# Kernel tuning notes

Measured on AMD Instinct MI355X. Metric: run time of the kernel, lower is better.

The kernel has to match this reference:

```python
import jax, jax.numpy as jnp
import numpy as np


def setup_inputs() -> dict:
    key = jax.random.key(0)
    k1, k2, k3 = jax.random.split(key, 3)
    N, S = 65536, 128  # rays, samples per ray
    # t: sorted sample distances along each ray (near=2.0, far=6.0 typical NeRF bounds)
    t = jnp.sort(jax.random.uniform(k1, (N, S, 1), jnp.float32, 2.0, 6.0), axis=-2)
    # sigma: non-negative densities (post-ReLU/softplus output of NerfDensity)
    sigma = jax.random.uniform(k2, (N, S, 1), jnp.float32, 0.0, 2.0)
    # color: RGB in [0,1] (post-sigmoid output of NerfColor)
    color = jax.random.uniform(k3, (N, S, 3), jnp.float32, 0.0, 1.0)
    return {"t": t, "sigma": sigma, "color": color}


def integrate_ray(t, sigma, color, infinite=False):
    # t, sigma: [N, S, 1]; color: [N, S, 3]
    dt = t[..., 1:, :] - t[..., :-1, :]                      # [N, S-1, 1]
    last = 1e10 * jnp.ones_like(dt[..., 0:1, :]) if infinite else jnp.zeros_like(dt[..., 0:1, :])
    dt = jnp.concatenate((dt, last), axis=-2)                # [N, S, 1]
    sdt = sigma * dt                                         # [N, S, 1]
    Ti = jnp.exp(-jnp.cumsum(sdt, axis=-2))[..., 0:-1, :]    # transmittance, shifted
    Ti = jnp.concatenate((jnp.ones_like(Ti[..., 0:1, :]), Ti), axis=-2)
    alpha = 1.0 - jnp.exp(-sdt)
    wi = Ti * alpha                                          # [N, S, 1]
    return ((wi * color).sum(axis=-2), (wi * t).sum(axis=-2), wi, t)


def reference(t, sigma, color):
    # forward(): t is sorted along the sample dim before integration.
    t = jnp.sort(t, axis=-2)
    return integrate_ray(t, sigma, color, infinite=False)
```

## Files before the change

### kernel.cpp

```cpp
#include <hip/hip_runtime.h>
#include <math.h>


#define NRAYS 65536
#define S 128
#define RAYS_PER_BLOCK 8

typedef float __attribute__((ext_vector_type(4))) fvec4;

__global__ __launch_bounds__(256) void nerf_render_kernel(
    const float* __restrict__ t,
    const float* __restrict__ sigma,
    const float* __restrict__ color,
    float* __restrict__ out_color,
    float* __restrict__ out_depth,
    float* __restrict__ out_wi,
    float* __restrict__ out_t)
{
    const int lane    = threadIdx.x & 63;
    const int seglane = lane & 31;
    const int wave    = threadIdx.x >> 6;
    const int ray = blockIdx.x * RAYS_PER_BLOCK + wave * 2 + (lane >> 5);

    const long sbase = (long)ray * S + 4 * seglane;

    const fvec4 tv = *(const fvec4*)(t + sbase);
    const fvec4 sv = *(const fvec4*)(sigma + sbase);
    const fvec4* cp = (const fvec4*)(color + (long)ray * (S * 3) + 12 * seglane);
    const fvec4 c0 = cp[0];
    const fvec4 c1 = cp[1];
    const fvec4 c2 = cp[2];

    const float t_next = __shfl_down(tv.x, 1, 32);
    const float dt0 = tv.y - tv.x;
    const float dt1 = tv.z - tv.y;
    const float dt2 = tv.w - tv.z;
    const float dt3 = (seglane == 31) ? 0.0f : (t_next - tv.w);

    const float p0  = sv.x * dt0;
    const float p1  = p0 + sv.y * dt1;
    const float p2  = p1 + sv.z * dt2;
    const float tot = p2 + sv.w * dt3;

    float scan = tot;
    #pragma unroll
    for (int off = 1; off < 32; off <<= 1) {
        const float v = __shfl_up(scan, off, 32);
        if (seglane >= off) scan += v;
    }
    const float excl = scan - tot;

    const float E0 = expf(-excl);
    const float e0 = expf(-(excl + p0));
    const float e1 = expf(-(excl + p1));
    const float e2 = expf(-(excl + p2));
    const float e3 = expf(-scan);
    const float wi0 = E0 - e0;
    const float wi1 = e0 - e1;
    const float wi2 = e1 - e2;
    const float wi3 = e2 - e3;

    fvec4 wiv; wiv.x = wi0; wiv.y = wi1; wiv.z = wi2; wiv.w = wi3;
    __builtin_nontemporal_store(wiv, (fvec4*)(out_wi + sbase));
    __builtin_nontemporal_store(tv,  (fvec4*)(out_t + sbase));

    float r = wi0 * c0.x + wi1 * c0.w + wi2 * c1.z + wi3 * c2.y;
    float g = wi0 * c0.y + wi1 * c1.x + wi2 * c1.w + wi3 * c2.z;
    float b = wi0 * c0.z + wi1 * c1.y + wi2 * c2.x + wi3 * c2.w;
    float d = wi0 * tv.x + wi1 * tv.y + wi2 * tv.z + wi3 * tv.w;

    #pragma unroll
    for (int off = 16; off >= 1; off >>= 1) {
        r += __shfl_xor(r, off, 32);
        g += __shfl_xor(g, off, 32);
        b += __shfl_xor(b, off, 32);
        d += __shfl_xor(d, off, 32);
    }

    if (seglane == 0) {
        out_color[(long)ray * 3 + 0] = r;
        out_color[(long)ray * 3 + 1] = g;
        out_color[(long)ray * 3 + 2] = b;
        out_depth[ray] = d;
    }
}

extern "C" void kernel_launch(void* const* d_in, const int* in_sizes, int n_in,
                              void* d_out, int out_size, void* d_ws, size_t ws_size,
                              hipStream_t stream) {
    const float* t     = (const float*)d_in[0];
    const float* sigma = (const float*)d_in[1];
    const float* color = (const float*)d_in[2];

    float* out = (float*)d_out;
    float* out_color = out;
    float* out_depth = out_color + (long)NRAYS * 3;
    float* out_wi    = out_depth + NRAYS;
    float* out_t     = out_wi + (long)NRAYS * S;

    const int blocks = NRAYS / RAYS_PER_BLOCK;
    nerf_render_kernel<<<blocks, 256, 0, stream>>>(
        t, sigma, color, out_color, out_depth, out_wi, out_t);
}
```

Measured before the change: 214.1 us.

## Use persistent grid-stride blocks with register prefetch of next ray batch

The launch shrinks from 8192 blocks to 2048 blocks, and each block now loops over 4 batches of rays. Inside the loop it prefetches the next batch's t, sigma and color into registers while the current batch is computed, hiding load latency. It also switches expf to the fast __expf intrinsic. The cost is more register use and fewer resident waves, which could cut memory-level parallelism on a bandwidth-bound kernel, plus slightly lower exp accuracy.

```diff
diff --git a/kernel.cpp b/kernel.cpp
--- a/kernel.cpp
+++ b/kernel.cpp
@@ -4,7 +4,9 @@
 
 #define NRAYS 65536
 #define S 128
-#define RAYS_PER_BLOCK 8
+#define BLOCKS 2048
+#define RAYS_PER_ITER 8
+#define ITERS (NRAYS / (BLOCKS * RAYS_PER_ITER))
 
 typedef float __attribute__((ext_vector_type(4))) fvec4;
 
@@ -20,68 +22,86 @@
     const int lane    = threadIdx.x & 63;
     const int seglane = lane & 31;
     const int wave    = threadIdx.x >> 6;
-    const int ray = blockIdx.x * RAYS_PER_BLOCK + wave * 2 + (lane >> 5);
+    const int seg     = lane >> 5;
 
-    const long sbase = (long)ray * S + 4 * seglane;
+    const int sub = wave * 2 + seg;
 
-    const fvec4 tv = *(const fvec4*)(t + sbase);
-    const fvec4 sv = *(const fvec4*)(sigma + sbase);
+    int ray = (0 * BLOCKS + blockIdx.x) * RAYS_PER_ITER + sub;
+    long sbase = (long)ray * S + 4 * seglane;
+    fvec4 tv = *(const fvec4*)(t + sbase);
+    fvec4 sv = *(const fvec4*)(sigma + sbase);
     const fvec4* cp = (const fvec4*)(color + (long)ray * (S * 3) + 12 * seglane);
-    const fvec4 c0 = cp[0];
-    const fvec4 c1 = cp[1];
-    const fvec4 c2 = cp[2];
-
-    const float t_next = __shfl_down(tv.x, 1, 32);
-    const float dt0 = tv.y - tv.x;
-    const float dt1 = tv.z - tv.y;
-    const float dt2 = tv.w - tv.z;
-    const float dt3 = (seglane == 31) ? 0.0f : (t_next - tv.w);
-
-    const float p0  = sv.x * dt0;
-    const float p1  = p0 + sv.y * dt1;
-    const float p2  = p1 + sv.z * dt2;
-    const float tot = p2 + sv.w * dt3;
-
-    float scan = tot;
-    #pragma unroll
-    for (int off = 1; off < 32; off <<= 1) {
-        const float v = __shfl_up(scan, off, 32);
-        if (seglane >= off) scan += v;
-    }
-    const float excl = scan - tot;
-
-    const float E0 = expf(-excl);
-    const float e0 = expf(-(excl + p0));
-    const float e1 = expf(-(excl + p1));
-    const float e2 = expf(-(excl + p2));
-    const float e3 = expf(-scan);
-    const float wi0 = E0 - e0;
-    const float wi1 = e0 - e1;
-    const float wi2 = e1 - e2;
-    const float wi3 = e2 - e3;
-
-    fvec4 wiv; wiv.x = wi0; wiv.y = wi1; wiv.z = wi2; wiv.w = wi3;
-    __builtin_nontemporal_store(wiv, (fvec4*)(out_wi + sbase));
-    __builtin_nontemporal_store(tv,  (fvec4*)(out_t + sbase));
-
-    float r = wi0 * c0.x + wi1 * c0.w + wi2 * c1.z + wi3 * c2.y;
-    float g = wi0 * c0.y + wi1 * c1.x + wi2 * c1.w + wi3 * c2.z;
-    float b = wi0 * c0.z + wi1 * c1.y + wi2 * c2.x + wi3 * c2.w;
-    float d = wi0 * tv.x + wi1 * tv.y + wi2 * tv.z + wi3 * tv.w;
+    fvec4 c0 = cp[0], c1 = cp[1], c2 = cp[2];
 
     #pragma unroll
-    for (int off = 16; off >= 1; off >>= 1) {
-        r += __shfl_xor(r, off, 32);
-        g += __shfl_xor(g, off, 32);
-        b += __shfl_xor(b, off, 32);
-        d += __shfl_xor(d, off, 32);
-    }
+    for (int it = 0; it < ITERS; ++it) {
+        fvec4 ntv, nsv, nc0, nc1, nc2;
+        long nsbase = 0;
+        if (it + 1 < ITERS) {
+            const int nray = ((it + 1) * BLOCKS + blockIdx.x) * RAYS_PER_ITER + sub;
+            nsbase = (long)nray * S + 4 * seglane;
+            ntv = *(const fvec4*)(t + nsbase);
+            nsv = *(const fvec4*)(sigma + nsbase);
+            const fvec4* ncp = (const fvec4*)(color + (long)nray * (S * 3) + 12 * seglane);
+            nc0 = ncp[0]; nc1 = ncp[1]; nc2 = ncp[2];
+        }
 
-    if (seglane == 0) {
-        out_color[(long)ray * 3 + 0] = r;
-        out_color[(long)ray * 3 + 1] = g;
-        out_color[(long)ray * 3 + 2] = b;
-        out_depth[ray] = d;
+        const float t_next = __shfl_down(tv.x, 1, 32);
+        const float dt0 = tv.y - tv.x;
+        const float dt1 = tv.z - tv.y;
+        const float dt2 = tv.w - tv.z;
+        const float dt3 = (seglane == 31) ? 0.0f : (t_next - tv.w);
+
+        const float p0  = sv.x * dt0;
+        const float p1  = p0 + sv.y * dt1;
+        const float p2  = p1 + sv.z * dt2;
+        const float tot = p2 + sv.w * dt3;
+
+        float scan = tot;
+        #pragma unroll
+        for (int off = 1; off < 32; off <<= 1) {
+            const float v = __shfl_up(scan, off, 32);
+            if (seglane >= off) scan += v;
+        }
+        const float excl = scan - tot;
+
+        const float E0 = __expf(-excl);
+        const float e0 = __expf(-(excl + p0));
+        const float e1 = __expf(-(excl + p1));
+        const float e2 = __expf(-(excl + p2));
+        const float e3 = __expf(-scan);
+        const float wi0 = E0 - e0;
+        const float wi1 = e0 - e1;
+        const float wi2 = e1 - e2;
+        const float wi3 = e2 - e3;
+
+        fvec4 wiv; wiv.x = wi0; wiv.y = wi1; wiv.z = wi2; wiv.w = wi3;
+        __builtin_nontemporal_store(wiv, (fvec4*)(out_wi + sbase));
+        __builtin_nontemporal_store(tv,  (fvec4*)(out_t + sbase));
+
+        float r = wi0 * c0.x + wi1 * c0.w + wi2 * c1.z + wi3 * c2.y;
+        float g = wi0 * c0.y + wi1 * c1.x + wi2 * c1.w + wi3 * c2.z;
+        float b = wi0 * c0.z + wi1 * c1.y + wi2 * c2.x + wi3 * c2.w;
+        float d = wi0 * tv.x + wi1 * tv.y + wi2 * tv.z + wi3 * tv.w;
+
+        #pragma unroll
+        for (int off = 16; off >= 1; off >>= 1) {
+            r += __shfl_xor(r, off, 32);
+            g += __shfl_xor(g, off, 32);
+            b += __shfl_xor(b, off, 32);
+            d += __shfl_xor(d, off, 32);
+        }
+
+        if (seglane == 0) {
+            out_color[(long)ray * 3 + 0] = r;
+            out_color[(long)ray * 3 + 1] = g;
+            out_color[(long)ray * 3 + 2] = b;
+            out_depth[ray] = d;
+        }
+
+        ray = ((it + 1) * BLOCKS + blockIdx.x) * RAYS_PER_ITER + sub;
+        sbase = nsbase;
+        tv = ntv; sv = nsv; c0 = nc0; c1 = nc1; c2 = nc2;
     }
 }
 
@@ -98,7 +118,6 @@
     float* out_wi    = out_depth + NRAYS;
     float* out_t     = out_wi + (long)NRAYS * S;
 
-    const int blocks = NRAYS / RAYS_PER_BLOCK;
-    nerf_render_kernel<<<blocks, 256, 0, stream>>>(
+    nerf_render_kernel<<<BLOCKS, 256, 0, stream>>>(
         t, sigma, color, out_color, out_depth, out_wi, out_t);
 }
```

Result: no change. 216.9 us (+1.3%).

## Split t passthrough copy into separate kernel and use fast exp

Applied to the files above, without the earlier changes.

Moves the copy of t into the output into its own grid-stride copy kernel launched before the integration kernel, and removes that store from the integration kernel. It also replaces expf with __expf. The intent is to simplify the main kernel's store stream. The cost is reading t a second time from memory plus an extra kernel launch, and __expf trades some accuracy.

```diff
diff --git a/kernel.cpp b/kernel.cpp
--- a/kernel.cpp
+++ b/kernel.cpp
@@ -8,14 +8,13 @@
 
 typedef float __attribute__((ext_vector_type(4))) fvec4;
 
-__global__ __launch_bounds__(256) void nerf_render_kernel(
+__global__ __launch_bounds__(256) void nerf_integrate_kernel(
     const float* __restrict__ t,
     const float* __restrict__ sigma,
     const float* __restrict__ color,
     float* __restrict__ out_color,
     float* __restrict__ out_depth,
-    float* __restrict__ out_wi,
-    float* __restrict__ out_t)
+    float* __restrict__ out_wi)
 {
     const int lane    = threadIdx.x & 63;
     const int seglane = lane & 31;
@@ -50,11 +49,11 @@
     }
     const float excl = scan - tot;
 
-    const float E0 = expf(-excl);
-    const float e0 = expf(-(excl + p0));
-    const float e1 = expf(-(excl + p1));
-    const float e2 = expf(-(excl + p2));
-    const float e3 = expf(-scan);
+    const float E0 = __expf(-excl);
+    const float e0 = __expf(-(excl + p0));
+    const float e1 = __expf(-(excl + p1));
+    const float e2 = __expf(-(excl + p2));
+    const float e3 = __expf(-scan);
     const float wi0 = E0 - e0;
     const float wi1 = e0 - e1;
     const float wi2 = e1 - e2;
@@ -62,7 +61,6 @@
 
     fvec4 wiv; wiv.x = wi0; wiv.y = wi1; wiv.z = wi2; wiv.w = wi3;
     __builtin_nontemporal_store(wiv, (fvec4*)(out_wi + sbase));
-    __builtin_nontemporal_store(tv,  (fvec4*)(out_t + sbase));
 
     float r = wi0 * c0.x + wi1 * c0.w + wi2 * c1.z + wi3 * c2.y;
     float g = wi0 * c0.y + wi1 * c1.x + wi2 * c1.w + wi3 * c2.z;
@@ -85,6 +83,24 @@
     }
 }
 
+#define COPY_BLOCKS 2048
+#define COPY_VEC4   (NRAYS * S / 4)
+
+__global__ __launch_bounds__(256) void nerf_tcopy_kernel(
+    const float* __restrict__ t,
+    float* __restrict__ out_t)
+{
+    const fvec4* src = (const fvec4*)t;
+    fvec4* dst = (fvec4*)out_t;
+    const int stride = COPY_BLOCKS * 256;
+    int idx = blockIdx.x * 256 + threadIdx.x;
+    #pragma unroll
+    for (int i = 0; i < COPY_VEC4 / (COPY_BLOCKS * 256); ++i) {
+        __builtin_nontemporal_store(src[idx], dst + idx);
+        idx += stride;
+    }
+}
+
 extern "C" void kernel_launch(void* const* d_in, const int* in_sizes, int n_in,
                               void* d_out, int out_size, void* d_ws, size_t ws_size,
                               hipStream_t stream) {
@@ -98,7 +114,9 @@
     float* out_wi    = out_depth + NRAYS;
     float* out_t     = out_wi + (long)NRAYS * S;
 
+    nerf_tcopy_kernel<<<COPY_BLOCKS, 256, 0, stream>>>(t, out_t);
+
     const int blocks = NRAYS / RAYS_PER_BLOCK;
-    nerf_render_kernel<<<blocks, 256, 0, stream>>>(
-        t, sigma, color, out_color, out_depth, out_wi, out_t);
+    nerf_integrate_kernel<<<blocks, 256, 0, stream>>>(
+        t, sigma, color, out_color, out_depth, out_wi);
 }
```

After: 214.9 us. Within noise of the previous version (+0.4%).
